# Kernel tuning notes

Hardware: AMD Instinct MI355X
Metric: run time of the kernel (lower is better)

The kernel has to match this reference:

```python
import math
import jax, jax.numpy as jnp
import numpy as np

HIDDEN = 1024
N_HEADS = 16
HEAD_DIM = HIDDEN // N_HEADS
SEQ = 2048
BATCH = 2
MAX_SEQ = 2048
N_LAYERS = 4
ALPHA = 0.3
TOPK_FACTOR = 2
GAMMA = 0.5
M_FREQ = math.ceil(MAX_SEQ / 2) + 1  # rfft length


def _sample_indices(layer_idx):
    # FrequencyRampSampler.get_sample_indices (layer_idx is a static python int)
    l = layer_idx + 1
    M, L = M_FREQ, N_LAYERS
    if ALPHA > 1.0 / L:
        p = int(M * (1 - ALPHA) * (1 - (l - 1) / (L - 1))) if L > 1 else 0
        q = int(p + ALPHA * M)
    else:
        p = int(M * (1 - l / L))
        q = int(p + M / L)
    p = max(0, min(p, M - 1))
    q = max(p + 1, min(q, M))
    return p, q


def setup_inputs() -> dict:
    key = jax.random.key(0)
    ks = jax.random.split(key, 10)
    hidden_states = jax.random.normal(ks[0], (BATCH, SEQ, HIDDEN), jnp.float32)
    # causal additive mask [B,1,N,N]
    causal = jnp.tril(jnp.ones((SEQ, SEQ), jnp.float32))
    attention_mask = jnp.where(causal > 0, 0.0, -1e9).astype(jnp.float32)
    attention_mask = jnp.broadcast_to(attention_mask[None, None], (BATCH, 1, SEQ, SEQ))
    s = 0.02
    Wq = jax.random.normal(ks[1], (HIDDEN, HIDDEN), jnp.float32) * s
    Wk = jax.random.normal(ks[2], (HIDDEN, HIDDEN), jnp.float32) * s
    Wv = jax.random.normal(ks[3], (HIDDEN, HIDDEN), jnp.float32) * s
    Wo = jax.random.normal(ks[4], (HIDDEN, HIDDEN), jnp.float32) * s
    bq = jnp.zeros((HIDDEN,), jnp.float32)
    bk = jnp.zeros((HIDDEN,), jnp.float32)
    bv = jnp.zeros((HIDDEN,), jnp.float32)
    bo = jnp.zeros((HIDDEN,), jnp.float32)
    return dict(hidden_states=hidden_states, attention_mask=attention_mask,
                Wq=Wq, bq=bq, Wk=Wk, bk=bk, Wv=Wv, bv=bv, Wo=Wo, bo=bo,
                layer_idx=1)


def _forward(hidden_states, attention_mask, Wq, bq, Wk, bk, Wv, bv, Wo, bo, layer_idx):
    B, N, D = hidden_states.shape
    p, q = _sample_indices(layer_idx)
    Q = hidden_states @ Wq.T + bq
    K = hidden_states @ Wk.T + bk
    V = hidden_states @ Wv.T + bv

    # ---- time-domain branch: FFT -> band-select -> IFFT -> SDPA ----
    def band_filter(X):
        Xf = jnp.fft.rfft(X, axis=1)  # [B, M, D] complex64
        Xp = jnp.zeros_like(Xf).at[:, p:q, :].set(Xf[:, p:q, :])
        return jnp.fft.irfft(Xp, n=N, axis=1)

    Qt = band_filter(Q).reshape(B, N, N_HEADS, HEAD_DIM).transpose(0, 2, 1, 3)
    Kt = band_filter(K).reshape(B, N, N_HEADS, HEAD_DIM).transpose(0, 2, 1, 3)
    Vt = band_filter(V).reshape(B, N, N_HEADS, HEAD_DIM).transpose(0, 2, 1, 3)
    scores = jnp.einsum('bhnd,bhmd->bhnm', Qt, Kt) / math.sqrt(HEAD_DIM)
    scores = scores + attention_mask
    probs = jax.nn.softmax(scores, axis=-1)
    time_out = jnp.einsum('bhnm,bhmd->bhnd', probs, Vt)
    time_out = time_out.transpose(0, 2, 1, 3).reshape(B, N, D)

    # ---- frequency-domain branch: autocorrelation + top-k delay aggregation ----
    Qf = jnp.fft.rfft(Q, axis=1)
    Kf = jnp.fft.rfft(K, axis=1)
    corr = jnp.zeros_like(Qf).at[:, p:q, :].set(Qf[:, p:q, :] * jnp.conj(Kf[:, p:q, :]))
    R = jnp.fft.irfft(corr, n=N, axis=1)          # [B, N, D]
    R_mean = R.mean(axis=-1)                       # [B, N]
    k = min(max(1, int(TOPK_FACTOR * math.log(N + 1))), N)
    top_R, top_idx = jax.lax.top_k(R_mean, k)      # [B, k]
    attn_w = jax.nn.softmax(top_R, axis=-1)        # [B, k]
    # rolled index: (n - tau) mod N, for each of the k delays
    idx = (jnp.arange(N)[None, None, :] - top_idx[:, :, None]) % N   # [B, k, N]
    gathered = jnp.take_along_axis(V[:, None, :, :], idx[..., None], axis=2)  # [B, k, N, D]
    freq_out = jnp.einsum('bk,bknd->bnd', attn_w, gathered)

    out = GAMMA * time_out + (1.0 - GAMMA) * freq_out
    return out @ Wo.T + bo


def reference(hidden_states, attention_mask, Wq, bq, Wk, bk, Wv, bv, Wo, bo, layer_idx):
    return _forward(hidden_states, attention_mask, Wq, bq, Wk, bk, Wv, bv, Wo, bo, layer_idx)
```

## Files before the change

kernel.cpp:

```cpp
#include <hip/hip_runtime.h>
#include <hip/hip_bf16.h>

#define BATCHN 2
#define SEQ    2048
#define HID    1024
#define NHEADS 16
#define HD     64
#define P_LO   478
#define NF     307
#define NF2    614
#define NFP    640
#define KTOP   15
#define DPI    3.14159265358979323846

typedef __bf16 bf16_t;
typedef bf16_t v8bf __attribute__((ext_vector_type(8)));
typedef bf16_t v4bf __attribute__((ext_vector_type(4)));
typedef float  v4f  __attribute__((ext_vector_type(4)));

#define MFMA(a,b,c) __builtin_amdgcn_mfma_f32_16x16x32_bf16(a,b,c,0,0,0)

#define GLDS(gp, lp) __builtin_amdgcn_global_load_lds( \
    (const __attribute__((address_space(1))) void*)(gp), \
    (__attribute__((address_space(3))) void*)(lp), 16, 0, 0)

__launch_bounds__(256)
__global__ void detect_kernel(const unsigned short* __restrict__ x0,
                              const unsigned short* __restrict__ x1,
                              int* __restrict__ flag) {
    int t = threadIdx.x, bad = 0;
    for (int i = t; i < 8192; i += 256) {
        unsigned e0 = (x0[i] >> 7) & 0xFF; if (e0 >= 0x90) bad++;
        unsigned e1 = (x1[i] >> 7) & 0xFF; if (e1 >= 0x90) bad++;
    }
    __shared__ int s[256];
    s[t] = bad; __syncthreads();
    for (int st = 128; st; st >>= 1) { if (t < st) s[t] += s[t + st]; __syncthreads(); }
    if (t == 0) *flag = (s[0] > 64) ? 1 : 0;
}

__launch_bounds__(256)
__global__ void tab_kernel(bf16_t* __restrict__ Ahi, bf16_t* __restrict__ Alo,
                           bf16_t* __restrict__ Gt) {
    __shared__ float T[64 * 65];
    int t = threadIdx.x;
    int m0 = blockIdx.x * 64, r0 = blockIdx.y * 64;
    int m = t >> 2, rb = (t & 3) * 16;
    {
        v8bf g0, g1;
        #pragma unroll
        for (int i = 0; i < 16; i++) {
            int r = r0 + rb + i;
            float v = 0.f;
            if (r < NF2) {
                int f  = P_LO + (r < NF ? r : r - NF);
                int ph = (f * (m0 + m)) & (SEQ - 1);
                float ang = (float)(2.0 * DPI / SEQ) * (float)ph;
                float sn, cs;
                sincosf(ang, &sn, &cs);
                v = (r < NF) ? cs : sn;
            }
            T[(rb + i) * 65 + m] = v;
            bf16_t gv = (bf16_t)(v * (float)(2.0 / SEQ));
            if (i < 8) g0[i] = gv; else g1[i - 8] = gv;
        }
        *(v8bf*)&Gt[(size_t)(m0 + m) * NFP + r0 + rb]     = g0;
        *(v8bf*)&Gt[(size_t)(m0 + m) * NFP + r0 + rb + 8] = g1;
    }
    __syncthreads();
    int r = t >> 2, mb = (t & 3) * 16;
    v8bf h0, h1, l0, l1;
    #pragma unroll
    for (int i = 0; i < 16; i++) {
        float v = T[r * 65 + mb + i];
        bf16_t hh = (bf16_t)v;
        bf16_t ll = (bf16_t)(v - (float)hh);
        if (i < 8) { h0[i] = hh; l0[i] = ll; } else { h1[i - 8] = hh; l1[i - 8] = ll; }
    }
    size_t ro = (size_t)(r0 + r) * SEQ + m0 + mb;
    *(v8bf*)&Ahi[ro]     = h0;  *(v8bf*)&Ahi[ro + 8] = h1;
    *(v8bf*)&Alo[ro]     = l0;  *(v8bf*)&Alo[ro + 8] = l1;
}

__launch_bounds__(256)
__global__ void norm_x_kernel(const int* __restrict__ flag, const void* __restrict__ Xv,
                              bf16_t* __restrict__ Xh, bf16_t* __restrict__ XTh,
                              bf16_t* __restrict__ XTl) {
    int fl = *flag;
    __shared__ float T[64 * 65];
    int t = threadIdx.x;
    int R0 = blockIdx.y * 64, C0 = blockIdx.x * 64;
    int r = t >> 2;
    #pragma unroll
    for (int it = 0; it < 2; it++) {
        int c = (t & 3) * 8 + it * 32;
        float x[8];
        if (fl) {
            const float* p = (const float*)Xv + (size_t)(R0 + r) * HID + C0 + c;
            #pragma unroll
            for (int e = 0; e < 8; e++) x[e] = p[e];
        } else {
            const bf16_t* p = (const bf16_t*)Xv + (size_t)(R0 + r) * HID + C0 + c;
            #pragma unroll
            for (int e = 0; e < 8; e++) x[e] = (float)p[e];
        }
        v8bf h;
        #pragma unroll
        for (int e = 0; e < 8; e++) { h[e] = (bf16_t)x[e]; T[(r) * 65 + c + e] = x[e]; }
        *(v8bf*)&Xh[(size_t)(R0 + r) * HID + C0 + c] = h;
    }
    __syncthreads();
    int b  = blockIdx.y >> 5;
    int Rl = R0 - b * SEQ;
    int d  = t >> 2;
    #pragma unroll
    for (int it = 0; it < 2; it++) {
        int n = (t & 3) * 8 + it * 32;
        v8bf h, l;
        #pragma unroll
        for (int e = 0; e < 8; e++) {
            float x = T[(n + e) * 65 + d];
            bf16_t hh = (bf16_t)x;
            h[e] = hh; l[e] = (bf16_t)(x - (float)hh);
        }
        size_t off = ((size_t)b * HID + C0 + d) * SEQ + Rl + n;
        *(v8bf*)&XTh[off] = h;
        *(v8bf*)&XTl[off] = l;
    }
}

__launch_bounds__(256)
__global__ void gemm128_nt(const int* __restrict__ flag, const bf16_t* __restrict__ A,
                           const void* __restrict__ Braw, const void* __restrict__ biasraw,
                           void* __restrict__ Out, int outmode) {
    int fl = *flag;
    __shared__ __align__(16) bf16_t As[128 * 32];
    __shared__ __align__(16) bf16_t Bs[128 * 32];
    int t = threadIdx.x, wave = t >> 6, lane = t & 63;
    int lrow = lane & 15, quad = lane >> 4;
    int m0 = blockIdx.y * 128, n0 = blockIdx.x * 128;
    int wm = (wave >> 1) * 64, wn = (wave & 1) * 64;
    int grow = lane >> 2, gcol = (lane & 3) * 8;
    v4f acc[4][4] = {};
    for (int k0 = 0; k0 < HID; k0 += 32) {
        __syncthreads();
        GLDS(&A[(size_t)(m0 + wave * 32 + grow) * HID + k0 + gcol],      &As[(wave * 32) * 32]);
        GLDS(&A[(size_t)(m0 + wave * 32 + 16 + grow) * HID + k0 + gcol], &As[(wave * 32 + 16) * 32]);
        if (!fl) {
            const bf16_t* B = (const bf16_t*)Braw;
            GLDS(&B[(size_t)(n0 + wave * 32 + grow) * HID + k0 + gcol],      &Bs[(wave * 32) * 32]);
            GLDS(&B[(size_t)(n0 + wave * 32 + 16 + grow) * HID + k0 + gcol], &Bs[(wave * 32 + 16) * 32]);
        } else {
            const float* B = (const float*)Braw;
            #pragma unroll
            for (int i2 = 0; i2 < 2; i2++) {
                int row = (t >> 2) + 64 * i2, col = (t & 3) * 8;
                const float* p = &B[(size_t)(n0 + row) * HID + k0 + col];
                v8bf h;
                #pragma unroll
                for (int e = 0; e < 8; e++) h[e] = (bf16_t)p[e];
                *(v8bf*)&Bs[row * 32 + col] = h;
            }
        }
        __syncthreads();
        v8bf a[4], b[4];
        #pragma unroll
        for (int i = 0; i < 4; i++) a[i] = *(v8bf*)&As[(wm + i * 16 + lrow) * 32 + quad * 8];
        #pragma unroll
        for (int j = 0; j < 4; j++) b[j] = *(v8bf*)&Bs[(wn + j * 16 + lrow) * 32 + quad * 8];
        #pragma unroll
        for (int i = 0; i < 4; i++)
        #pragma unroll
        for (int j = 0; j < 4; j++) acc[i][j] = MFMA(a[i], b[j], acc[i][j]);
    }
    #pragma unroll
    for (int i = 0; i < 4; i++)
    #pragma unroll
    for (int j = 0; j < 4; j++) {
        int col = n0 + wn + 16 * j + lrow;
        float bvv = fl ? ((const float*)biasraw)[col] : (float)((const bf16_t*)biasraw)[col];
        #pragma unroll
        for (int rg = 0; rg < 4; rg++) {
            int row = m0 + wm + 16 * i + quad * 4 + rg;
            float v = acc[i][j][rg] + bvv;
            size_t off = (size_t)row * HID + col;
            if (outmode == 1 && fl) ((float*)Out)[off] = v;
            else ((bf16_t*)Out)[off] = (bf16_t)v;
        }
    }
}

__launch_bounds__(256)
__global__ void band_fwd(const bf16_t* __restrict__ Ahi, const bf16_t* __restrict__ Alo,
                         const bf16_t* __restrict__ XTh, const bf16_t* __restrict__ XTl,
                         bf16_t* __restrict__ Xfh, bf16_t* __restrict__ Xfl) {
    __shared__ __align__(16) bf16_t Ah[64 * 32], Al[64 * 32], Bh[64 * 32], Bl[64 * 32];
    int t = threadIdx.x, wave = t >> 6, lane = t & 63;
    int lrow = lane & 15, quad = lane >> 4;
    int m0 = blockIdx.y * 64, n0 = blockIdx.x * 64, b = blockIdx.z;
    int wm = (wave >> 1) * 32, wn = (wave & 1) * 32;
    int srow = t >> 2, scol = (t & 3) * 8;
    const bf16_t* bth = XTh + (size_t)b * HID * SEQ;
    const bf16_t* btl = XTl + (size_t)b * HID * SEQ;
    v4f acc[2][2] = {};
    for (int k0 = 0; k0 < SEQ; k0 += 32) {
        __syncthreads();
        GLDS(&Ahi[(size_t)(m0 + srow) * SEQ + k0 + scol], &Ah[srow * 32 + scol]);
        GLDS(&Alo[(size_t)(m0 + srow) * SEQ + k0 + scol], &Al[srow * 32 + scol]);
        GLDS(&bth[(size_t)(n0 + srow) * SEQ + k0 + scol], &Bh[srow * 32 + scol]);
        GLDS(&btl[(size_t)(n0 + srow) * SEQ + k0 + scol], &Bl[srow * 32 + scol]);
        __syncthreads();
        v8bf ah0 = *(v8bf*)&Ah[(wm + lrow) * 32 + quad * 8];
        v8bf ah1 = *(v8bf*)&Ah[(wm + 16 + lrow) * 32 + quad * 8];
        v8bf al0 = *(v8bf*)&Al[(wm + lrow) * 32 + quad * 8];
        v8bf al1 = *(v8bf*)&Al[(wm + 16 + lrow) * 32 + quad * 8];
        v8bf bh0 = *(v8bf*)&Bh[(wn + lrow) * 32 + quad * 8];
        v8bf bh1 = *(v8bf*)&Bh[(wn + 16 + lrow) * 32 + quad * 8];
        v8bf bl0 = *(v8bf*)&Bl[(wn + lrow) * 32 + quad * 8];
        v8bf bl1 = *(v8bf*)&Bl[(wn + 16 + lrow) * 32 + quad * 8];
        acc[0][0] = MFMA(ah0, bh0, acc[0][0]); acc[0][0] = MFMA(ah0, bl0, acc[0][0]); acc[0][0] = MFMA(al0, bh0, acc[0][0]);
        acc[0][1] = MFMA(ah0, bh1, acc[0][1]); acc[0][1] = MFMA(ah0, bl1, acc[0][1]); acc[0][1] = MFMA(al0, bh1, acc[0][1]);
        acc[1][0] = MFMA(ah1, bh0, acc[1][0]); acc[1][0] = MFMA(ah1, bl0, acc[1][0]); acc[1][0] = MFMA(al1, bh0, acc[1][0]);
        acc[1][1] = MFMA(ah1, bh1, acc[1][1]); acc[1][1] = MFMA(ah1, bl1, acc[1][1]); acc[1][1] = MFMA(al1, bh1, acc[1][1]);
    }
    bf16_t* oh = Xfh + (size_t)b * NFP * HID;
    bf16_t* ol = Xfl + (size_t)b * NFP * HID;
    #pragma unroll
    for (int i = 0; i < 2; i++)
    #pragma unroll
    for (int j = 0; j < 2; j++) {
        int col = n0 + wn + 16 * j + lrow;
        #pragma unroll
        for (int rg = 0; rg < 4; rg++) {
            int row = m0 + wm + 16 * i + quad * 4 + rg;
            float v = acc[i][j][rg];
            bf16_t h = (bf16_t)v;
            oh[(size_t)row * HID + col] = h;
            ol[(size_t)row * HID + col] = (bf16_t)(v - (float)h);
        }
    }
}

__launch_bounds__(256)
__global__ void proj_f(const int* __restrict__ flag, const bf16_t* __restrict__ Xfh,
                       const bf16_t* __restrict__ Xfl,
                       const void* __restrict__ Wq_, const void* __restrict__ Wk_,
                       const void* __restrict__ Wv_,
                       bf16_t* __restrict__ Qfh, bf16_t* __restrict__ Qfl,
                       bf16_t* __restrict__ Kfh, bf16_t* __restrict__ Kfl,
                       bf16_t* __restrict__ QfT, bf16_t* __restrict__ KfT,
                       bf16_t* __restrict__ VfT) {
    int fl = *flag;
    int bz = blockIdx.z, b = bz & 1, sel = bz >> 1;
    const void* Wraw = sel == 0 ? Wq_ : sel == 1 ? Wk_ : Wv_;
    bf16_t* Ch = sel == 0 ? Qfh : Kfh;
    bf16_t* Cl = sel == 0 ? Qfl : Kfl;
    bf16_t* CT = sel == 0 ? QfT : sel == 1 ? KfT : VfT;
    bool qk = sel < 2;
    __shared__ __align__(16) bf16_t Ah[64 * 32], Al[64 * 32], Bh[64 * 32], Bl[64 * 32];
    int t = threadIdx.x, wave = t >> 6, lane = t & 63;
    int lrow = lane & 15, quad = lane >> 4;
    int m0 = blockIdx.y * 64, n0 = blockIdx.x * 64;
    int wm = (wave >> 1) * 32, wn = (wave & 1) * 32;
    int srow = t >> 2, scol = (t & 3) * 8;
    const size_t zo = (size_t)b * NFP * HID;
    v4f acc[2][2] = {};
    for (int k0 = 0; k0 < HID; k0 += 32) {
        __syncthreads();
        GLDS(&Xfh[zo + (size_t)(m0 + srow) * HID + k0 + scol], &Ah[srow * 32 + scol]);
        GLDS(&Xfl[zo + (size_t)(m0 + srow) * HID + k0 + scol], &Al[srow * 32 + scol]);
        {
            float xb[8];
            if (fl) {
                const float* p = (const float*)Wraw + (size_t)(n0 + srow) * HID + k0 + scol;
                #pragma unroll
                for (int e = 0; e < 8; e++) xb[e] = p[e];
            } else {
                const bf16_t* p = (const bf16_t*)Wraw + (size_t)(n0 + srow) * HID + k0 + scol;
                #pragma unroll
                for (int e = 0; e < 8; e++) xb[e] = (float)p[e];
            }
            v8bf h, l;
            #pragma unroll
            for (int e = 0; e < 8; e++) {
                bf16_t hh = (bf16_t)xb[e];
                h[e] = hh; l[e] = (bf16_t)(xb[e] - (float)hh);
            }
            *(v8bf*)&Bh[srow * 32 + scol] = h;
            *(v8bf*)&Bl[srow * 32 + scol] = l;
        }
        __syncthreads();
        v8bf ah0 = *(v8bf*)&Ah[(wm + lrow) * 32 + quad * 8];
        v8bf ah1 = *(v8bf*)&Ah[(wm + 16 + lrow) * 32 + quad * 8];
        v8bf al0 = *(v8bf*)&Al[(wm + lrow) * 32 + quad * 8];
        v8bf al1 = *(v8bf*)&Al[(wm + 16 + lrow) * 32 + quad * 8];
        v8bf bh0 = *(v8bf*)&Bh[(wn + lrow) * 32 + quad * 8];
        v8bf bh1 = *(v8bf*)&Bh[(wn + 16 + lrow) * 32 + quad * 8];
        acc[0][0] = MFMA(ah0, bh0, acc[0][0]); acc[0][0] = MFMA(al0, bh0, acc[0][0]);
        acc[0][1] = MFMA(ah0, bh1, acc[0][1]); acc[0][1] = MFMA(al0, bh1, acc[0][1]);
        acc[1][0] = MFMA(ah1, bh0, acc[1][0]); acc[1][0] = MFMA(al1, bh0, acc[1][0]);
        acc[1][1] = MFMA(ah1, bh1, acc[1][1]); acc[1][1] = MFMA(al1, bh1, acc[1][1]);
        if (qk) {
            v8bf bl0 = *(v8bf*)&Bl[(wn + lrow) * 32 + quad * 8];
            v8bf bl1 = *(v8bf*)&Bl[(wn + 16 + lrow) * 32 + quad * 8];
            acc[0][0] = MFMA(ah0, bl0, acc[0][0]);
            acc[0][1] = MFMA(ah0, bl1, acc[0][1]);
            acc[1][0] = MFMA(ah1, bl0, acc[1][0]);
            acc[1][1] = MFMA(ah1, bl1, acc[1][1]);
        }
    }
    #pragma unroll
    for (int i = 0; i < 2; i++)
    #pragma unroll
    for (int j = 0; j < 2; j++) {
        int col = n0 + wn + 16 * j + lrow;
        v4bf pk;
        #pragma unroll
        for (int rg = 0; rg < 4; rg++) {
            int row = m0 + wm + 16 * i + quad * 4 + rg;
            float v = acc[i][j][rg];
            bf16_t h = (bf16_t)v;
            pk[rg] = h;
            if (qk) {
                Ch[zo + (size_t)row * HID + col] = h;
                Cl[zo + (size_t)row * HID + col] = (bf16_t)(v - (float)h);
            }
        }
        *(v4bf*)&CT[zo + (size_t)col * NFP + m0 + wm + 16 * i + quad * 4] = pk;
    }
}

__launch_bounds__(256)
__global__ void inv128_f(const bf16_t* __restrict__ Gt, const bf16_t* __restrict__ QfT,
                         const bf16_t* __restrict__ KfT, const bf16_t* __restrict__ VfT,
                         bf16_t* __restrict__ Qt, bf16_t* __restrict__ Kt,
                         bf16_t* __restrict__ VTd) {
    int bz = blockIdx.z, b = bz & 1, sel = bz >> 1;
    const bf16_t* BT = (sel == 0 ? QfT : sel == 1 ? KfT : VfT) + (size_t)b * HID * NFP;
    bf16_t* Out = sel == 0 ? Qt : sel == 1 ? Kt : VTd;
    bool trans = (sel == 2);
    __shared__ __align__(16) bf16_t As[128 * 32];
    __shared__ __align__(16) bf16_t Bs[128 * 32];
    int t = threadIdx.x, wave = t >> 6, lane = t & 63;
    int lrow = lane & 15, quad = lane >> 4;
    int m0 = blockIdx.y * 128, n0 = blockIdx.x * 128;
    int wm = (wave >> 1) * 64, wn = (wave & 1) * 64;
    int grow = lane >> 2, gcol = (lane & 3) * 8;
    v4f acc[4][4] = {};
    for (int k0 = 0; k0 < NFP; k0 += 32) {
        __syncthreads();
        GLDS(&Gt[(size_t)(m0 + wave * 32 + grow) * NFP + k0 + gcol],      &As[(wave * 32) * 32]);
        GLDS(&Gt[(size_t)(m0 + wave * 32 + 16 + grow) * NFP + k0 + gcol], &As[(wave * 32 + 16) * 32]);
        GLDS(&BT[(size_t)(n0 + wave * 32 + grow) * NFP + k0 + gcol],      &Bs[(wave * 32) * 32]);
        GLDS(&BT[(size_t)(n0 + wave * 32 + 16 + grow) * NFP + k0 + gcol], &Bs[(wave * 32 + 16) * 32]);
        __syncthreads();
        v8bf a[4], bfr[4];
        #pragma unroll
        for (int i = 0; i < 4; i++) a[i]   = *(v8bf*)&As[(wm + i * 16 + lrow) * 32 + quad * 8];
        #pragma unroll
        for (int j = 0; j < 4; j++) bfr[j] = *(v8bf*)&Bs[(wn + j * 16 + lrow) * 32 + quad * 8];
        #pragma unroll
        for (int i = 0; i < 4; i++)
        #pragma unroll
        for (int j = 0; j < 4; j++) acc[i][j] = MFMA(a[i], bfr[j], acc[i][j]);
    }
    #pragma unroll
    for (int i = 0; i < 4; i++)
    #pragma unroll
    for (int j = 0; j < 4; j++) {
        int col = n0 + wn + 16 * j + lrow;
        if (trans) {
            v4bf pk;
            #pragma unroll
            for (int rg = 0; rg < 4; rg++) pk[rg] = (bf16_t)acc[i][j][rg];
            *(v4bf*)&Out[((size_t)b * HID + col) * SEQ + m0 + wm + 16 * i + quad * 4] = pk;
        } else {
            #pragma unroll
            for (int rg = 0; rg < 4; rg++) {
                int row = m0 + wm + 16 * i + quad * 4 + rg;
                Out[(size_t)b * SEQ * HID + (size_t)row * HID + col] = (bf16_t)acc[i][j][rg];
            }
        }
    }
}

__launch_bounds__(256)
__global__ void attn_kernel(const bf16_t* __restrict__ Qt, const bf16_t* __restrict__ Kt,
                            const bf16_t* __restrict__ VT, bf16_t* __restrict__ TO) {
    __shared__ __align__(16) bf16_t Ks[2][64 * 72];
    __shared__ __align__(16) bf16_t Vs[2][64 * 72];
    __shared__ __align__(16) bf16_t Ps[4 * 16 * 72];
    int t = threadIdx.x, wave = t >> 6, lane = t & 63;
    int lrow = lane & 15, quad = lane >> 4;
    int h = blockIdx.y, b = blockIdx.z;
    int q0 = (gridDim.x - 1 - blockIdx.x) * 64;
    const size_t base = (size_t)b * SEQ * HID + (size_t)h * HD;
    const bf16_t* vb_ = VT + ((size_t)b * HID + h * HD) * SEQ;
    bf16_t* Pw = &Ps[wave * 16 * 72];

    int qrow = q0 + wave * 16 + lrow;
    v8bf qa0 = *(const v8bf*)&Qt[base + (size_t)qrow * HID + quad * 8];
    v8bf qa1 = *(const v8bf*)&Qt[base + (size_t)qrow * HID + 32 + quad * 8];

    v4f o[4] = {};
    float m_i = -1e30f, l_i = 0.f;
    int qloc = wave * 16 + lrow;
    int srow = t >> 2, cc0 = (t & 3) * 16;
    int nch = q0 / 64 + 1;
    v8bf kp0 = *(const v8bf*)&Kt[base + (size_t)srow * HID + cc0];
    v8bf kp1 = *(const v8bf*)&Kt[base + (size_t)srow * HID + cc0 + 8];
    v8bf vp0 = *(const v8bf*)&vb_[(size_t)srow * SEQ + cc0];
    v8bf vp1 = *(const v8bf*)&vb_[(size_t)srow * SEQ + cc0 + 8];
    for (int c = 0; c < nch; c++) {
        int kb = c * 64;
        int cur = c & 1;
        bool masked = (kb == q0);
        *(v8bf*)&Ks[cur][srow * 72 + cc0]     = kp0;
        *(v8bf*)&Ks[cur][srow * 72 + cc0 + 8] = kp1;
        *(v8bf*)&Vs[cur][srow * 72 + cc0]     = vp0;
        *(v8bf*)&Vs[cur][srow * 72 + cc0 + 8] = vp1;
        __syncthreads();
        if (c + 1 < nch) {
            int kb2 = kb + 64;
            kp0 = *(const v8bf*)&Kt[base + (size_t)(kb2 + srow) * HID + cc0];
            kp1 = *(const v8bf*)&Kt[base + (size_t)(kb2 + srow) * HID + cc0 + 8];
            vp0 = *(const v8bf*)&vb_[(size_t)srow * SEQ + kb2 + cc0];
            vp1 = *(const v8bf*)&vb_[(size_t)srow * SEQ + kb2 + cc0 + 8];
        }
        v4f s[4];
        #pragma unroll
        for (int ct = 0; ct < 4; ct++) {
            v8bf kA0 = *(v8bf*)&Ks[cur][(ct * 16 + lrow) * 72 + quad * 8];
            v8bf kA1 = *(v8bf*)&Ks[cur][(ct * 16 + lrow) * 72 + 32 + quad * 8];
            v4f z = {};
            z = MFMA(kA0, qa0, z);
            s[ct] = MFMA(kA1, qa1, z);
        }
        float sv[4][4];
        float mx = -1e30f;
        #pragma unroll
        for (int ct = 0; ct < 4; ct++)
        #pragma unroll
        for (int r = 0; r < 4; r++) {
            float x = s[ct][r] * 0.125f;
            if (masked && (ct * 16 + quad * 4 + r > qloc)) x = -1e30f;
            sv[ct][r] = x;
            mx = fmaxf(mx, x);
        }
        mx = fmaxf(mx, __shfl_xor(mx, 16));
        mx = fmaxf(mx, __shfl_xor(mx, 32));
        float mnew = fmaxf(m_i, mx);
        float alpha = __expf(m_i - mnew);
        m_i = mnew;
        float rs = 0.f;
        #pragma unroll
        for (int ct = 0; ct < 4; ct++)
        #pragma unroll
        for (int r = 0; r < 4; r++) { float p = __expf(sv[ct][r] - mnew); sv[ct][r] = p; rs += p; }
        rs += __shfl_xor(rs, 16);
        rs += __shfl_xor(rs, 32);
        l_i = l_i * alpha + rs;
        #pragma unroll
        for (int r = 0; r < 4; r++) {
            float ar = __shfl(alpha, quad * 4 + r);
            #pragma unroll
            for (int dt = 0; dt < 4; dt++) o[dt][r] *= ar;
        }
        #pragma unroll
        for (int ct = 0; ct < 4; ct++) {
            v4bf pk;
            #pragma unroll
            for (int r = 0; r < 4; r++) pk[r] = (bf16_t)sv[ct][r];
            *(v4bf*)&Pw[lrow * 72 + ct * 16 + quad * 4] = pk;
        }
        v8bf pa0 = *(v8bf*)&Pw[lrow * 72 + quad * 8];
        v8bf pa1 = *(v8bf*)&Pw[lrow * 72 + 32 + quad * 8];
        #pragma unroll
        for (int dt = 0; dt < 4; dt++) {
            v8bf vb0 = *(v8bf*)&Vs[cur][(dt * 16 + lrow) * 72 + quad * 8];
            v8bf vb1 = *(v8bf*)&Vs[cur][(dt * 16 + lrow) * 72 + 32 + quad * 8];
            o[dt] = MFMA(pa0, vb0, o[dt]);
            o[dt] = MFMA(pa1, vb1, o[dt]);
        }
    }
    #pragma unroll
    for (int r = 0; r < 4; r++) {
        float lr = __shfl(l_i, quad * 4 + r);
        int qg = q0 + wave * 16 + quad * 4 + r;
        #pragma unroll
        for (int dt = 0; dt < 4; dt++)
            TO[base + (size_t)qg * HID + dt * 16 + lrow] = (bf16_t)(o[dt][r] / lr);
    }
}

__launch_bounds__(256)
__global__ void sfreq_kernel(const bf16_t* __restrict__ Qh, const bf16_t* __restrict__ Ql,
                             const bf16_t* __restrict__ Kh, const bf16_t* __restrict__ Kl,
                             float* __restrict__ Sre, float* __restrict__ Sim) {
    int f = blockIdx.x, b = blockIdx.y, t = threadIdx.x;
    const size_t oc = ((size_t)b * NFP + f) * HID;
    const size_t os = ((size_t)b * NFP + NF + f) * HID;
    float re = 0.f, im = 0.f;
    for (int d = t; d < HID; d += 256) {
        float cq = (float)Qh[oc + d] + (float)Ql[oc + d];
        float sq = (float)Qh[os + d] + (float)Ql[os + d];
        float ck = (float)Kh[oc + d] + (float)Kl[oc + d];
        float sk = (float)Kh[os + d] + (float)Kl[os + d];
        re += cq * ck + sq * sk;
        im += cq * sk - sq * ck;
    }
    #pragma unroll
    for (int msk = 1; msk < 64; msk <<= 1) { re += __shfl_xor(re, msk); im += __shfl_xor(im, msk); }
    __shared__ float rbuf[8];
    int wave = t >> 6, lane = t & 63;
    if (lane == 0) { rbuf[wave] = re; rbuf[4 + wave] = im; }
    __syncthreads();
    if (t == 0) {
        Sre[b * NF + f] = rbuf[0] + rbuf[1] + rbuf[2] + rbuf[3];
        Sim[b * NF + f] = rbuf[4] + rbuf[5] + rbuf[6] + rbuf[7];
    }
}

__launch_bounds__(256)
__global__ void rmean_kernel(const float* __restrict__ Sre, const float* __restrict__ Sim,
                             float* __restrict__ Rm) {
    int b = blockIdx.y;
    int nl = threadIdx.x & 63, part = threadIdx.x >> 6;
    int n = blockIdx.x * 64 + nl;
    __shared__ float sr[NF], si[NF];
    __shared__ float red[4][64];
    for (int i = threadIdx.x; i < NF; i += 256) { sr[i] = Sre[b * NF + i]; si[i] = Sim[b * NF + i]; }
    __syncthreads();
    float acc = 0.f;
    for (int r = part; r < NF; r += 4) {
        int ph = ((P_LO + r) * n) & (SEQ - 1);
        float ang = (float)(2.0 * DPI / SEQ) * (float)ph;
        float sn, cs;
        sincosf(ang, &sn, &cs);
        acc += sr[r] * cs - si[r] * sn;
    }
    red[part][nl] = acc;
    __syncthreads();
    if (part == 0) {
        float s = red[0][nl] + red[1][nl] + red[2][nl] + red[3][nl];
        Rm[b * SEQ + n] = s * (float)(2.0 / ((double)SEQ * (double)HID));
    }
}

__launch_bounds__(64)
__global__ void topk_kernel(const float* __restrict__ Rm, int* __restrict__ Ti,
                            float* __restrict__ Tw) {
    int b = blockIdx.x, lane = threadIdx.x;
    float v[32];
    #pragma unroll
    for (int j = 0; j < 32; j++) v[j] = Rm[b * SEQ + j * 64 + lane];
    float selv[KTOP];
    int   seli[KTOP];
    for (int kk = 0; kk < KTOP; kk++) {
        float best = -INFINITY; int bi = lane;
        #pragma unroll
        for (int j = 0; j < 32; j++) {
            float x = v[j];
            if (x > best) { best = x; bi = j * 64 + lane; }
        }
        #pragma unroll
        for (int off = 1; off < 64; off <<= 1) {
            float ov = __shfl_xor(best, off);
            int   oi = __shfl_xor(bi, off);
            if (ov > best || (ov == best && oi < bi)) { best = ov; bi = oi; }
        }
        selv[kk] = best; seli[kk] = bi;
        if (lane == (bi & 63)) v[bi >> 6] = -INFINITY;
    }
    float mx = selv[0];
    #pragma unroll
    for (int i = 1; i < KTOP; i++) mx = fmaxf(mx, selv[i]);
    float s = 0.f, e[KTOP];
    #pragma unroll
    for (int i = 0; i < KTOP; i++) { e[i] = __expf(selv[i] - mx); s += e[i]; }
    if (lane < KTOP) { Tw[b * KTOP + lane] = e[lane] / s; Ti[b * KTOP + lane] = seli[lane]; }
}

__launch_bounds__(256)
__global__ void combine_kernel(const bf16_t* __restrict__ TO, const bf16_t* __restrict__ V,
                               const int* __restrict__ Ti, const float* __restrict__ Tw,
                               bf16_t* __restrict__ Yc) {
    int b = blockIdx.z, n = blockIdx.y;
    int d = blockIdx.x * 256 + threadIdx.x;
    __shared__ int   ti[KTOP];
    __shared__ float tw[KTOP];
    if (threadIdx.x < KTOP) { ti[threadIdx.x] = Ti[b * KTOP + threadIdx.x]; tw[threadIdx.x] = Tw[b * KTOP + threadIdx.x]; }
    __syncthreads();
    float fo = 0.f;
    #pragma unroll
    for (int kk = 0; kk < KTOP; kk++) {
        int nn = (n - ti[kk] + SEQ) & (SEQ - 1);
        fo += tw[kk] * (float)V[((size_t)b * SEQ + nn) * HID + d];
    }
    size_t off = ((size_t)b * SEQ + n) * HID + d;
    Yc[off] = (bf16_t)(0.5f * (float)TO[off] + 0.5f * fo);
}

extern "C" void kernel_launch(void* const* d_in, const int* in_sizes, int n_in,
                              void* d_out, int out_size, void* d_ws, size_t ws_size,
                              hipStream_t stream) {
    (void)in_sizes; (void)n_in; (void)out_size; (void)ws_size;
    const void* X  = d_in[0];
    const void* Wq = d_in[2];
    const void* Wk = d_in[4];
    const void* Wv = d_in[6];
    const void* bv = d_in[7];
    const void* Wo = d_in[8];
    const void* bo = d_in[9];

    const size_t SZ_X   = (size_t)BATCHN * SEQ * HID * 2;
    const size_t SZ_TAB = (size_t)NFP * SEQ * 2;
    const size_t SZ_F   = (size_t)BATCHN * NFP * HID * 2;
    char* w = (char*)d_ws;
    bf16_t* Xh  = (bf16_t*)(w);
    bf16_t* Xfh = (bf16_t*)(w);
    bf16_t* Xfl = (bf16_t*)(w + SZ_F);
    bf16_t* Qt  = (bf16_t*)(w);
    bf16_t* Yc  = (bf16_t*)(w);
    bf16_t* XTh = (bf16_t*)(w + SZ_X);
    bf16_t* Qfh = (bf16_t*)(w + SZ_X);
    bf16_t* Qfl = (bf16_t*)(w + SZ_X + SZ_F);
    bf16_t* Kfh = (bf16_t*)(w + SZ_X + 2 * SZ_F);
    bf16_t* Kt  = (bf16_t*)(w + SZ_X);
    bf16_t* XTl = (bf16_t*)(w + 2 * SZ_X);
    bf16_t* Kfl = (bf16_t*)(w + 2 * SZ_X);
    bf16_t* QfT = (bf16_t*)(w + 2 * SZ_X + SZ_F);
    bf16_t* KfT = (bf16_t*)(w + 2 * SZ_X + 2 * SZ_F);
    bf16_t* TO  = (bf16_t*)(w + 2 * SZ_X);
    bf16_t* Vm  = (bf16_t*)(w + 3 * SZ_X);
    bf16_t* Gt  = (bf16_t*)(w + 4 * SZ_X);
    bf16_t* Ahi = (bf16_t*)(w + 4 * SZ_X + SZ_TAB);
    bf16_t* Alo = (bf16_t*)(w + 4 * SZ_X + 2 * SZ_TAB);
    bf16_t* VfT = (bf16_t*)(w + 4 * SZ_X + SZ_TAB);
    char*  sm  = w + 4 * SZ_X + 3 * SZ_TAB;
    int*   flag = (int*)sm;
    float* Sre  = (float*)(sm + 256);
    float* Sim  = (float*)(sm + 256 + 4096);
    float* Rm   = (float*)(sm + 256 + 8192);
    int*   Ti   = (int*)  (sm + 256 + 8192 + 16384);
    float* Tw   = (float*)(sm + 256 + 8192 + 16384 + 256);
    bf16_t* VT  = (bf16_t*)d_out;

    detect_kernel<<<1, 256, 0, stream>>>((const unsigned short*)X, (const unsigned short*)Wq, flag);
    tab_kernel<<<dim3(SEQ / 64, NFP / 64), 256, 0, stream>>>(Ahi, Alo, Gt);
    norm_x_kernel<<<dim3(16, 64), 256, 0, stream>>>(flag, X, Xh, XTh, XTl);
    gemm128_nt<<<dim3(8, 32), 256, 0, stream>>>(flag, Xh, Wv, bv, Vm, 0);
    band_fwd<<<dim3(16, NFP / 64, BATCHN), 256, 0, stream>>>(Ahi, Alo, XTh, XTl, Xfh, Xfl);
    proj_f<<<dim3(16, NFP / 64, 6), 256, 0, stream>>>(flag, Xfh, Xfl, Wq, Wk, Wv,
                                                      Qfh, Qfl, Kfh, Kfl, QfT, KfT, VfT);
    sfreq_kernel<<<dim3(NF, BATCHN), 256, 0, stream>>>(Qfh, Qfl, Kfh, Kfl, Sre, Sim);
    rmean_kernel<<<dim3(SEQ / 64, BATCHN), 256, 0, stream>>>(Sre, Sim, Rm);
    topk_kernel<<<BATCHN, 64, 0, stream>>>(Rm, Ti, Tw);
    inv128_f<<<dim3(8, 16, 6), 256, 0, stream>>>(Gt, QfT, KfT, VfT, Qt, Kt, VT);
    attn_kernel<<<dim3(SEQ / 64, NHEADS, BATCHN), 256, 0, stream>>>(Qt, Kt, VT, TO);
    combine_kernel<<<dim3(HID / 256, SEQ, BATCHN), 256, 0, stream>>>(TO, Vm, Ti, Tw, Yc);
    gemm128_nt<<<dim3(8, 32), 256, 0, stream>>>(flag, Yc, Wo, bo, d_out, 1);
}
```

Before: 437.1 us.

## Process two query tiles per attention block to reuse K/V chunk loads

Each attention block now handles 128 query rows (two 64-row groups) instead of 64. Every K/V chunk staged in shared memory is reused by both groups, and K/V fragments are loaded into registers once per chunk. This roughly halves K/V global traffic and the number of blocks. The cost is higher register pressure, an extra barrier per chunk, and half as many blocks, which may reduce occupancy and worsen load balance under the causal mask.

```diff
diff --git a/kernel.cpp b/kernel.cpp
--- a/kernel.cpp
+++ b/kernel.cpp
@@ -393,20 +393,22 @@
     int t = threadIdx.x, wave = t >> 6, lane = t & 63;
     int lrow = lane & 15, quad = lane >> 4;
     int h = blockIdx.y, b = blockIdx.z;
-    int q0 = (gridDim.x - 1 - blockIdx.x) * 64;
+    int q0 = (gridDim.x - 1 - blockIdx.x) * 128;
     const size_t base = (size_t)b * SEQ * HID + (size_t)h * HD;
     const bf16_t* vb_ = VT + ((size_t)b * HID + h * HD) * SEQ;
     bf16_t* Pw = &Ps[wave * 16 * 72];
 
-    int qrow = q0 + wave * 16 + lrow;
-    v8bf qa0 = *(const v8bf*)&Qt[base + (size_t)qrow * HID + quad * 8];
-    v8bf qa1 = *(const v8bf*)&Qt[base + (size_t)qrow * HID + 32 + quad * 8];
-
-    v4f o[4] = {};
-    float m_i = -1e30f, l_i = 0.f;
-    int qloc = wave * 16 + lrow;
+    v8bf qa[2][2];
+    #pragma unroll
+    for (int g = 0; g < 2; g++) {
+        int qrow = q0 + g * 64 + wave * 16 + lrow;
+        qa[g][0] = *(const v8bf*)&Qt[base + (size_t)qrow * HID + quad * 8];
+        qa[g][1] = *(const v8bf*)&Qt[base + (size_t)qrow * HID + 32 + quad * 8];
+    }
+    v4f o[2][4] = {};
+    float m_i[2] = {-1e30f, -1e30f}, l_i[2] = {0.f, 0.f};
     int srow = t >> 2, cc0 = (t & 3) * 16;
-    int nch = q0 / 64 + 1;
+    int nch = q0 / 64 + 2;
     v8bf kp0 = *(const v8bf*)&Kt[base + (size_t)srow * HID + cc0];
     v8bf kp1 = *(const v8bf*)&Kt[base + (size_t)srow * HID + cc0 + 8];
     v8bf vp0 = *(const v8bf*)&vb_[(size_t)srow * SEQ + cc0];
@@ -414,7 +416,6 @@
     for (int c = 0; c < nch; c++) {
         int kb = c * 64;
         int cur = c & 1;
-        bool masked = (kb == q0);
         *(v8bf*)&Ks[cur][srow * 72 + cc0]     = kp0;
         *(v8bf*)&Ks[cur][srow * 72 + cc0 + 8] = kp1;
         *(v8bf*)&Vs[cur][srow * 72 + cc0]     = vp0;
@@ -427,69 +428,81 @@
             vp0 = *(const v8bf*)&vb_[(size_t)srow * SEQ + kb2 + cc0];
             vp1 = *(const v8bf*)&vb_[(size_t)srow * SEQ + kb2 + cc0 + 8];
         }
-        v4f s[4];
+        v8bf kA[4][2], vB[4][2];
         #pragma unroll
         for (int ct = 0; ct < 4; ct++) {
-            v8bf kA0 = *(v8bf*)&Ks[cur][(ct * 16 + lrow) * 72 + quad * 8];
-            v8bf kA1 = *(v8bf*)&Ks[cur][(ct * 16 + lrow) * 72 + 32 + quad * 8];
-            v4f z = {};
-            z = MFMA(kA0, qa0, z);
-            s[ct] = MFMA(kA1, qa1, z);
-        }
-        float sv[4][4];
-        float mx = -1e30f;
-        #pragma unroll
-        for (int ct = 0; ct < 4; ct++)
-        #pragma unroll
-        for (int r = 0; r < 4; r++) {
-            float x = s[ct][r] * 0.125f;
-            if (masked && (ct * 16 + quad * 4 + r > qloc)) x = -1e30f;
-            sv[ct][r] = x;
-            mx = fmaxf(mx, x);
-        }
-        mx = fmaxf(mx, __shfl_xor(mx, 16));
-        mx = fmaxf(mx, __shfl_xor(mx, 32));
-        float mnew = fmaxf(m_i, mx);
-        float alpha = __expf(m_i - mnew);
-        m_i = mnew;
-        float rs = 0.f;
-        #pragma unroll
-        for (int ct = 0; ct < 4; ct++)
-        #pragma unroll
-        for (int r = 0; r < 4; r++) { float p = __expf(sv[ct][r] - mnew); sv[ct][r] = p; rs += p; }
-        rs += __shfl_xor(rs, 16);
-        rs += __shfl_xor(rs, 32);
-        l_i = l_i * alpha + rs;
-        #pragma unroll
-        for (int r = 0; r < 4; r++) {
-            float ar = __shfl(alpha, quad * 4 + r);
-            #pragma unroll
-            for (int dt = 0; dt < 4; dt++) o[dt][r] *= ar;
-        }
-        #pragma unroll
-        for (int ct = 0; ct < 4; ct++) {
-            v4bf pk;
-            #pragma unroll
-            for (int r = 0; r < 4; r++) pk[r] = (bf16_t)sv[ct][r];
-            *(v4bf*)&Pw[lrow * 72 + ct * 16 + quad * 4] = pk;
-        }
-        v8bf pa0 = *(v8bf*)&Pw[lrow * 72 + quad * 8];
-        v8bf pa1 = *(v8bf*)&Pw[lrow * 72 + 32 + quad * 8];
-        #pragma unroll
-        for (int dt = 0; dt < 4; dt++) {
-            v8bf vb0 = *(v8bf*)&Vs[cur][(dt * 16 + lrow) * 72 + quad * 8];
-            v8bf vb1 = *(v8bf*)&Vs[cur][(dt * 16 + lrow) * 72 + 32 + quad * 8];
-            o[dt] = MFMA(pa0, vb0, o[dt]);
-            o[dt] = MFMA(pa1, vb1, o[dt]);
-        }
-    }
+            kA[ct][0] = *(v8bf*)&Ks[cur][(ct * 16 + lrow) * 72 + quad * 8];
+            kA[ct][1] = *(v8bf*)&Ks[cur][(ct * 16 + lrow) * 72 + 32 + quad * 8];
+            vB[ct][0] = *(v8bf*)&Vs[cur][(ct * 16 + lrow) * 72 + quad * 8];
+            vB[ct][1] = *(v8bf*)&Vs[cur][(ct * 16 + lrow) * 72 + 32 + quad * 8];
+        }
+        #pragma unroll
+        for (int g = 0; g < 2; g++) {
+            if (kb >= q0 + g * 64 + 64) continue;
+            bool masked = (kb == q0 + g * 64);
+            v4f s[4];
+            #pragma unroll
+            for (int ct = 0; ct < 4; ct++) {
+                v4f z = {};
+                z = MFMA(kA[ct][0], qa[g][0], z);
+                s[ct] = MFMA(kA[ct][1], qa[g][1], z);
+            }
+            float sv[4][4];
+            float mx = -1e30f;
+            #pragma unroll
+            for (int ct = 0; ct < 4; ct++)
+            #pragma unroll
+            for (int r = 0; r < 4; r++) {
+                float x = s[ct][r] * 0.125f;
+                if (masked && (ct * 16 + quad * 4 + r > wave * 16 + lrow)) x = -1e30f;
+                sv[ct][r] = x;
+                mx = fmaxf(mx, x);
+            }
+            mx = fmaxf(mx, __shfl_xor(mx, 16));
+            mx = fmaxf(mx, __shfl_xor(mx, 32));
+            float mnew = fmaxf(m_i[g], mx);
+            float alpha = __expf(m_i[g] - mnew);
+            m_i[g] = mnew;
+            float rs = 0.f;
+            #pragma unroll
+            for (int ct = 0; ct < 4; ct++)
+            #pragma unroll
+            for (int r = 0; r < 4; r++) { float p = __expf(sv[ct][r] - mnew); sv[ct][r] = p; rs += p; }
+            rs += __shfl_xor(rs, 16);
+            rs += __shfl_xor(rs, 32);
+            l_i[g] = l_i[g] * alpha + rs;
+            #pragma unroll
+            for (int r = 0; r < 4; r++) {
+                float ar = __shfl(alpha, quad * 4 + r);
+                #pragma unroll
+                for (int dt = 0; dt < 4; dt++) o[g][dt][r] *= ar;
+            }
+            #pragma unroll
+            for (int ct = 0; ct < 4; ct++) {
+                v4bf pk;
+                #pragma unroll
+                for (int r = 0; r < 4; r++) pk[r] = (bf16_t)sv[ct][r];
+                *(v4bf*)&Pw[lrow * 72 + ct * 16 + quad * 4] = pk;
+            }
+            v8bf pa0 = *(v8bf*)&Pw[lrow * 72 + quad * 8];
+            v8bf pa1 = *(v8bf*)&Pw[lrow * 72 + 32 + quad * 8];
+            #pragma unroll
+            for (int dt = 0; dt < 4; dt++) {
+                o[g][dt] = MFMA(pa0, vB[dt][0], o[g][dt]);
+                o[g][dt] = MFMA(pa1, vB[dt][1], o[g][dt]);
+            }
+        }
+        __syncthreads();
+    }
+    #pragma unroll
+    for (int g = 0; g < 2; g++)
     #pragma unroll
     for (int r = 0; r < 4; r++) {
-        float lr = __shfl(l_i, quad * 4 + r);
-        int qg = q0 + wave * 16 + quad * 4 + r;
+        float lr = __shfl(l_i[g], quad * 4 + r);
+        int qg = q0 + g * 64 + wave * 16 + quad * 4 + r;
         #pragma unroll
         for (int dt = 0; dt < 4; dt++)
-            TO[base + (size_t)qg * HID + dt * 16 + lrow] = (bf16_t)(o[dt][r] / lr);
+            TO[base + (size_t)qg * HID + dt * 16 + lrow] = (bf16_t)(o[g][dt][r] / lr);
     }
 }
 
@@ -657,7 +670,7 @@
     rmean_kernel<<<dim3(SEQ / 64, BATCHN), 256, 0, stream>>>(Sre, Sim, Rm);
     topk_kernel<<<BATCHN, 64, 0, stream>>>(Rm, Ti, Tw);
     inv128_f<<<dim3(8, 16, 6), 256, 0, stream>>>(Gt, QfT, KfT, VfT, Qt, Kt, VT);
-    attn_kernel<<<dim3(SEQ / 64, NHEADS, BATCHN), 256, 0, stream>>>(Qt, Kt, VT, TO);
+    attn_kernel<<<dim3(SEQ / 128, NHEADS, BATCHN), 256, 0, stream>>>(Qt, Kt, VT, TO);
     combine_kernel<<<dim3(HID / 256, SEQ, BATCHN), 256, 0, stream>>>(TO, Vm, Ti, Tw, Yc);
     gemm128_nt<<<dim3(8, 32), 256, 0, stream>>>(flag, Yc, Wo, bo, d_out, 1);
 }
```

After: 433.7 us. Within noise of the previous version (-0.8%).
